# Kernel tuning notes

Measured on AMD Instinct MI355X. Metric: run time of the kernel, lower is better.

## Reference

```python
import jax, jax.numpy as jnp
import numpy as np

N_NODES = 100000
N_EDGES = 1600000
D_IN = 128
D_HID = 128
N_CLS = 2


def gcn_conv(x, edge_index, W, b):
    """PyG GCNConv: add self-loops, symmetric normalization, linear, scatter-add, bias."""
    n = x.shape[0]
    loop = jnp.arange(n, dtype=edge_index.dtype)
    src = jnp.concatenate([edge_index[0], loop])  # [E+N]
    dst = jnp.concatenate([edge_index[1], loop])
    # degree computed on destination (col) after adding self-loops
    deg = jax.ops.segment_sum(jnp.ones_like(dst, dtype=x.dtype), dst, num_segments=n)
    dinv = jnp.where(deg > 0, jax.lax.rsqrt(deg), 0.0)
    norm = dinv[src] * dinv[dst]  # [E+N]
    h = x @ W  # [N, out]
    msg = h[src] * norm[:, None]  # [E+N, out]
    out = jax.ops.segment_sum(msg, dst, num_segments=n)
    return out + b


def setup_inputs() -> dict:
    key = jax.random.key(0)
    k1, k2, k3, k4 = jax.random.split(key, 4)
    x = jax.random.normal(k1, (N_NODES, D_IN), dtype=jnp.float32)
    edge_index = jax.random.randint(k2, (2, N_EDGES), 0, N_NODES, dtype=jnp.int64)
    W1 = jax.random.normal(k3, (D_IN, D_HID), dtype=jnp.float32) * (1.0 / np.sqrt(D_IN))
    b1 = jnp.zeros((D_HID,), dtype=jnp.float32)
    W2 = jax.random.normal(k4, (D_HID, N_CLS), dtype=jnp.float32) * (1.0 / np.sqrt(D_HID))
    b2 = jnp.zeros((N_CLS,), dtype=jnp.float32)
    return {"x": x, "edge_index": edge_index, "W1": W1, "b1": b1, "W2": W2, "b2": b2}


def reference(x, edge_index, W1, b1, W2, b2):
    h = gcn_conv(x, edge_index, W1, b1)
    h = jax.nn.relu(h)
    # training=False -> dropout skipped
    out = gcn_conv(h, edge_index, W2, b2)
    return out
```

## Files before the change

kernel.cpp:

```cpp
#include <hip/hip_runtime.h>
#include <hip/hip_fp16.h>
#include <cstdint>
#include <cstddef>

#define NN 100000
#define NE 1600000
#define D 128
#define NBK 782
#define NBLK_P 200
#define EPB 8000
#define CAP 3072

typedef _Float16 half8 __attribute__((ext_vector_type(8)));
typedef _Float16 half4v __attribute__((ext_vector_type(4)));
typedef float f32x4 __attribute__((ext_vector_type(4)));


__launch_bounds__(256)
__global__ void pscat_k(const int* __restrict__ ei, unsigned* __restrict__ gcnt,
                        unsigned* __restrict__ part,
                        const float* __restrict__ W, _Float16* __restrict__ Wt) {
    __shared__ unsigned hist[NBK];
    __shared__ unsigned run[NBK];
    int tid = threadIdx.x, b = blockIdx.x;
    for (int k = tid; k < NBK; k += 256) hist[k] = 0u;
    __syncthreads();
    int e0 = b * EPB;
    for (int i = tid * 4; i < EPB; i += 1024) {
        int4 d4 = *(const int4*)(ei + NE + e0 + i);
        atomicAdd(&hist[d4.x >> 7], 1u);
        atomicAdd(&hist[d4.y >> 7], 1u);
        atomicAdd(&hist[d4.z >> 7], 1u);
        atomicAdd(&hist[d4.w >> 7], 1u);
    }
    __syncthreads();
    for (int k = tid; k < NBK; k += 256) {
        unsigned c = hist[k];
        run[k] = c ? atomicAdd(&gcnt[k * 16], c) : 0u;
    }
    if (b < 64) {
        int idx = b * 256 + tid;
        int n = idx >> 7, kk = idx & 127;
        Wt[idx] = (_Float16)W[kk * 128 + n];
    }
    __syncthreads();
    for (int i = tid * 4; i < EPB; i += 1024) {
        int4 s4 = *(const int4*)(ei + e0 + i);
        int4 d4 = *(const int4*)(ei + NE + e0 + i);
        unsigned k, slot;
        k = (unsigned)(d4.x >> 7); slot = atomicAdd(&run[k], 1u);
        if (slot < CAP) part[(size_t)k * CAP + slot] = (unsigned)s4.x | ((unsigned)(d4.x & 127) << 20);
        k = (unsigned)(d4.y >> 7); slot = atomicAdd(&run[k], 1u);
        if (slot < CAP) part[(size_t)k * CAP + slot] = (unsigned)s4.y | ((unsigned)(d4.y & 127) << 20);
        k = (unsigned)(d4.z >> 7); slot = atomicAdd(&run[k], 1u);
        if (slot < CAP) part[(size_t)k * CAP + slot] = (unsigned)s4.z | ((unsigned)(d4.z & 127) << 20);
        k = (unsigned)(d4.w >> 7); slot = atomicAdd(&run[k], 1u);
        if (slot < CAP) part[(size_t)k * CAP + slot] = (unsigned)s4.w | ((unsigned)(d4.w & 127) << 20);
    }
}

__global__ void pscan_k(const unsigned* __restrict__ gcnt, unsigned* __restrict__ base) {
    __shared__ unsigned sh[1024];
    int t = threadIdx.x;
    unsigned v = 0u;
    if (t < NBK) {
        v = gcnt[t * 16];
        if (v > CAP) v = CAP;
    }
    sh[t] = v;
    __syncthreads();
    for (int off = 1; off < 1024; off <<= 1) {
        unsigned u = (t >= off) ? sh[t - off] : 0u;
        __syncthreads();
        sh[t] += u;
        __syncthreads();
    }
    if (t < NBK) base[t] = sh[t] - v;
    if (t == NBK) base[NBK] = sh[NBK - 1];
}

__launch_bounds__(256)
__global__ void p4_csr_k(const unsigned* __restrict__ part, const unsigned* __restrict__ base,
                         unsigned* __restrict__ rp, float* __restrict__ dinv,
                         unsigned* __restrict__ col) {
    __shared__ unsigned c[128], p[128], run[128];
    int tid = threadIdx.x, k = blockIdx.x;
    int n0 = k << 7;
    int nodes = (NN - n0 < 128) ? (NN - n0) : 128;
    unsigned e0c = base[k], e1c = base[k + 1];
    unsigned cnt = e1c - e0c;
    const unsigned* pk = part + (size_t)k * CAP;

    if (tid < 128) c[tid] = 0u;
    __syncthreads();
    for (unsigned t = tid; t < cnt; t += 256)
        atomicAdd(&c[(pk[t] >> 20) & 127], 1u);
    __syncthreads();

    unsigned myc = (tid < 128) ? c[tid] : 0u;
    if (tid < 128) p[tid] = myc;
    __syncthreads();
    for (int off = 1; off < 128; off <<= 1) {
        unsigned u = 0;
        if (tid < 128 && tid >= off) u = p[tid - off];
        __syncthreads();
        if (tid < 128) p[tid] += u;
        __syncthreads();
    }
    if (tid < 128) {
        unsigned excl = p[tid] - myc;
        run[tid] = excl;
        if (tid < nodes) {
            rp[n0 + tid] = e0c + excl;
            dinv[n0 + tid] = rsqrtf((float)(myc + 1u));
        }
    }
    if (k == 0 && tid == 0) rp[NN] = base[NBK];
    __syncthreads();

    for (unsigned t = tid; t < cnt; t += 256) {
        unsigned v = pk[t];
        unsigned dlo = (v >> 20) & 127;
        unsigned pos = e0c + atomicAdd(&run[dlo], 1u);
        col[pos] = v & 0xFFFFFu;
    }
}

__launch_bounds__(256)
__global__ void gemm1_k(const float* __restrict__ x, const _Float16* __restrict__ Wt,
                        const float* __restrict__ dinv, _Float16* __restrict__ h) {
    __shared__ _Float16 wt[128 * 136];
    __shared__ _Float16 xs[128 * 72];
    int tid = threadIdx.x;
    int rb = blockIdx.x * 128;
    int w = tid >> 6, lane = tid & 63;
    int m = lane & 15, q4 = lane >> 4;

#pragma unroll
    for (int q = 0; q < 8; q++) {
        int idx = q * 256 + tid;
        int n = idx >> 4, k8 = (idx & 15) * 8;
        *(half8*)(&wt[n * 136 + k8]) = *(const half8*)(Wt + n * 128 + k8);
    }

    f32x4 acc[2][8];
#pragma unroll
    for (int rt = 0; rt < 2; rt++)
#pragma unroll
        for (int nt = 0; nt < 8; nt++) acc[rt][nt] = (f32x4){0.f, 0.f, 0.f, 0.f};

    for (int ks = 0; ks <= 64; ks += 64) {
        if (ks) __syncthreads();
#pragma unroll
        for (int q = 0; q < 8; q++) {
            int idx = q * 256 + tid;
            int row = idx >> 4;
            int c4 = (idx & 15) * 4;
            int gr = rb + row;
            float4 v = (gr < NN) ? *(const float4*)(x + (size_t)gr * 128 + ks + c4)
                                 : make_float4(0, 0, 0, 0);
            half4v hv = { (_Float16)v.x, (_Float16)v.y, (_Float16)v.z, (_Float16)v.w };
            *(half4v*)(&xs[row * 72 + c4]) = hv;
        }
        __syncthreads();

#pragma unroll
        for (int kc = 0; kc < 2; kc++) {
            half8 a0 = *(const half8*)(&xs[(w * 32 + m) * 72 + kc * 32 + q4 * 8]);
            half8 a1 = *(const half8*)(&xs[(w * 32 + 16 + m) * 72 + kc * 32 + q4 * 8]);
#pragma unroll
            for (int nt = 0; nt < 8; nt++) {
                half8 bf = *(const half8*)(&wt[(nt * 16 + m) * 136 + ks + kc * 32 + q4 * 8]);
                acc[0][nt] = __builtin_amdgcn_mfma_f32_16x16x32_f16(a0, bf, acc[0][nt], 0, 0, 0);
                acc[1][nt] = __builtin_amdgcn_mfma_f32_16x16x32_f16(a1, bf, acc[1][nt], 0, 0, 0);
            }
        }
    }

    float dv[2][4];
#pragma unroll
    for (int rt = 0; rt < 2; rt++)
#pragma unroll
        for (int r = 0; r < 4; r++) {
            int ri = rb + w * 32 + rt * 16 + q4 * 4 + r;
            dv[rt][r] = (ri < NN) ? dinv[ri] : 0.f;
        }
    __syncthreads();
#pragma unroll
    for (int rt = 0; rt < 2; rt++)
#pragma unroll
        for (int nt = 0; nt < 8; nt++)
#pragma unroll
            for (int r = 0; r < 4; r++)
                wt[(w * 32 + rt * 16 + q4 * 4 + r) * 136 + nt * 16 + m] =
                    (_Float16)(acc[rt][nt][r] * dv[rt][r]);
    __syncthreads();
#pragma unroll
    for (int q = 0; q < 8; q++) {
        int idx = q * 256 + tid;
        int row = idx >> 4;
        int c8 = (idx & 15) * 8;
        int gr = rb + row;
        if (gr < NN)
            *(half8*)(h + (size_t)gr * 128 + c8) = *(const half8*)(&wt[row * 136 + c8]);
    }
}

__launch_bounds__(256)
__global__ void agg1_k(const _Float16* __restrict__ h, const unsigned* __restrict__ rp,
                       const unsigned* __restrict__ col, const float* __restrict__ dinv,
                       const float* __restrict__ b1, const float* __restrict__ W2,
                       float* __restrict__ z, int nb, int ne) {
    int i = nb + ((blockIdx.x * 256 + threadIdx.x) >> 6);
    int lane = threadIdx.x & 63;
    if (i >= ne) return;
    unsigned si = __builtin_amdgcn_readfirstlane((unsigned)i);

    const __half2* hb = (const __half2*)h;
    unsigned p0 = __builtin_amdgcn_readfirstlane(rp[si]);
    unsigned p1 = __builtin_amdgcn_readfirstlane(rp[si + 1]);
    int deg = (int)(p1 - p0);

    unsigned cv = col[p0 + (unsigned)lane];

    int degc = deg > 64 ? 64 : deg;
    int R = (degc + 15) >> 4;
    float2 sv = __half22float2(hb[(size_t)si * 64u + lane]);
    float f = (float)(1 + degc - 16 * R);
    float ax = f * sv.x, ay = f * sv.y;

#define ROUND16(r)                                                           \
    {                                                                        \
        float2 vv[16];                                                       \
        _Pragma("unroll")                                                    \
        for (int t = 0; t < 16; t++) {                                       \
            int k = (r) * 16 + t;                                            \
            unsigned s = (k < degc) ? __builtin_amdgcn_readlane(cv, k) : si; \
            vv[t] = __half22float2(hb[(size_t)s * 64u + lane]);              \
        }                                                                    \
        ax += ((vv[0].x + vv[1].x) + (vv[2].x + vv[3].x))                    \
            + ((vv[4].x + vv[5].x) + (vv[6].x + vv[7].x))                    \
            + ((vv[8].x + vv[9].x) + (vv[10].x + vv[11].x))                  \
            + ((vv[12].x + vv[13].x) + (vv[14].x + vv[15].x));               \
        ay += ((vv[0].y + vv[1].y) + (vv[2].y + vv[3].y))                    \
            + ((vv[4].y + vv[5].y) + (vv[6].y + vv[7].y))                    \
            + ((vv[8].y + vv[9].y) + (vv[10].y + vv[11].y))                  \
            + ((vv[12].y + vv[13].y) + (vv[14].y + vv[15].y));               \
    }

    if (degc > 0)  ROUND16(0)
    if (degc > 16) ROUND16(1)
    if (degc > 32) ROUND16(2)
    if (degc > 48) ROUND16(3)
#undef ROUND16

    for (unsigned e = p0 + 64; e < p1; ++e) {
        unsigned s_ = __builtin_amdgcn_readfirstlane(col[e]);
        float2 v = __half22float2(hb[(size_t)s_ * 64u + lane]);
        ax += v.x;
        ay += v.y;
    }

    float di = dinv[si];
    ax *= di;
    ay *= di;

    float2 bv = ((const float2*)b1)[lane];
    float h0 = fmaxf(ax + bv.x, 0.f);
    float h1 = fmaxf(ay + bv.y, 0.f);

    float4 w = ((const float4*)W2)[lane];
    float pz0 = fmaf(h0, w.x, h1 * w.z);
    float pz1 = fmaf(h0, w.y, h1 * w.w);
#pragma unroll
    for (int off = 32; off > 0; off >>= 1) {
        pz0 += __shfl_down(pz0, off);
        pz1 += __shfl_down(pz1, off);
    }
    if (lane == 0) {
        float2* zp = (float2*)(z + (size_t)si * 2);
        *zp = make_float2(pz0 * di, pz1 * di);
    }
}

__launch_bounds__(256)
__global__ void agg2_k(const float* __restrict__ z, const unsigned* __restrict__ rp,
                       const unsigned* __restrict__ col, const float* __restrict__ dinv,
                       const float* __restrict__ b2, float* __restrict__ out) {
    int i = (blockIdx.x * 256 + threadIdx.x) >> 4;
    int sl = threadIdx.x & 15;
    if (i >= NN) return;

    unsigned p0 = rp[i], p1 = rp[i + 1];
    float a0 = 0.f, a1 = 0.f;
    for (unsigned e = p0 + sl; e < p1; e += 16) {
        unsigned s = col[e];
        float2 v = ((const float2*)z)[s];
        a0 += v.x;
        a1 += v.y;
    }
#pragma unroll
    for (int off = 8; off > 0; off >>= 1) {
        a0 += __shfl_down(a0, off, 16);
        a1 += __shfl_down(a1, off, 16);
    }
    if (sl == 0) {
        float di = dinv[i];
        float2 zi = ((const float2*)z)[i];
        out[(size_t)i * 2]     = (a0 + zi.x) * di + b2[0];
        out[(size_t)i * 2 + 1] = (a1 + zi.y) * di + b2[1];
    }
}

extern "C" void kernel_launch(void* const* d_in, const int* in_sizes, int n_in,
                              void* d_out, int out_size, void* d_ws, size_t ws_size,
                              hipStream_t stream) {
    const float* x  = (const float*)d_in[0];
    const int*   ei = (const int*)d_in[1];
    const float* W1 = (const float*)d_in[2];
    const float* b1 = (const float*)d_in[3];
    const float* W2 = (const float*)d_in[4];
    const float* b2 = (const float*)d_in[5];
    float* out = (float*)d_out;

    char* ws = (char*)d_ws;
    unsigned* part = (unsigned*)(ws);
    unsigned* gcnt = (unsigned*)(ws + 9609216);
    unsigned* base = (unsigned*)(ws + 9659264);
    _Float16* h    = (_Float16*)(ws);
    float*    z    = (float*)(ws + 25600000);
    float*    dinv = (float*)(ws + 26400000);
    unsigned* rp   = (unsigned*)(ws + 26800000);
    unsigned* col  = (unsigned*)(ws + 27200016);
    _Float16* Wt   = (_Float16*)(ws + 33600016);

    hipMemsetAsync(gcnt, 0, 782 * 16 * sizeof(unsigned), stream);
    pscat_k<<<NBLK_P, 256, 0, stream>>>(ei, gcnt, part, W1, Wt);
    pscan_k<<<1, 1024, 0, stream>>>(gcnt, base);
    p4_csr_k<<<NBK, 256, 0, stream>>>(part, base, rp, dinv, col);

    gemm1_k<<<(NN + 127) / 128, 256, 0, stream>>>(x, Wt, dinv, h);
    agg1_k<<<(50000 * 64 + 255) / 256, 256, 0, stream>>>(h, rp, col, dinv, b1, W2, z, 0, 50000);
    agg1_k<<<(50000 * 64 + 255) / 256, 256, 0, stream>>>(h, rp, col, dinv, b1, W2, z, 50000, NN);
    agg2_k<<<(NN * 16 + 255) / 256, 256, 0, stream>>>(z, rp, col, dinv, b2, out);
}
```

Before: 227.0 us.

## Split layer-1 aggregation across two feature halves with interleaved block mapping

The first-layer gather is restructured so that each wavefront handles only 64 of the 128 hidden features of a node, loading one half per lane instead of a half2. Block IDs are interleaved so that nearby blocks cover both halves of the same node group, keeping the gathered rows' cache lines hot. Each half writes its own partial layer-2 projection (z0, z1), and agg2 sums the two. This doubles the number of wavefronts and the neighbor-index work. It also replaces the two half-range launches with a single launch, aiming for more parallelism and better L2 locality. The cost is twice the z reads in agg2 and narrower 2-byte loads per lane.

```diff
diff --git a/kernel.cpp b/kernel.cpp
--- a/kernel.cpp
+++ b/kernel.cpp
@@ -207,16 +207,24 @@
 }
 
 __launch_bounds__(256)
-__global__ void agg1_k(const _Float16* __restrict__ h, const unsigned* __restrict__ rp,
-                       const unsigned* __restrict__ col, const float* __restrict__ dinv,
-                       const float* __restrict__ b1, const float* __restrict__ W2,
-                       float* __restrict__ z, int nb, int ne) {
-    int i = nb + ((blockIdx.x * 256 + threadIdx.x) >> 6);
+__global__ void agg1h_k(const _Float16* __restrict__ h, const unsigned* __restrict__ rp,
+                        const unsigned* __restrict__ col, const float* __restrict__ dinv,
+                        const float* __restrict__ b1, const float* __restrict__ W2,
+                        float* __restrict__ z0, float* __restrict__ z1) {
+    unsigned bid = blockIdx.x;
+    unsigned rr = bid & 7u, q = bid >> 3;
+    unsigned dh = rr >> 2;
+    unsigned g  = q * 4u + (rr & 3u);
+    int wv = threadIdx.x >> 6;
     int lane = threadIdx.x & 63;
-    if (i >= ne) return;
-    unsigned si = __builtin_amdgcn_readfirstlane((unsigned)i);
-
-    const __half2* hb = (const __half2*)h;
+    unsigned i = g * 4u + (unsigned)wv;
+    if (i >= NN) return;
+    unsigned si = __builtin_amdgcn_readfirstlane(i);
+
+    const __half* hh = (const __half*)h;
+    unsigned doff = dh * 64u + (unsigned)lane;
+    const __half* hd = hh + doff;
+
     unsigned p0 = __builtin_amdgcn_readfirstlane(rp[si]);
     unsigned p1 = __builtin_amdgcn_readfirstlane(rp[si + 1]);
     int deg = (int)(p1 - p0);
@@ -225,27 +233,23 @@
 
     int degc = deg > 64 ? 64 : deg;
     int R = (degc + 15) >> 4;
-    float2 sv = __half22float2(hb[(size_t)si * 64u + lane]);
+    float sv = __half2float(hd[(size_t)si * 128u]);
     float f = (float)(1 + degc - 16 * R);
-    float ax = f * sv.x, ay = f * sv.y;
+    float ax = f * sv;
 
 #define ROUND16(r)                                                           \
     {                                                                        \
-        float2 vv[16];                                                       \
+        float vv[16];                                                        \
         _Pragma("unroll")                                                    \
         for (int t = 0; t < 16; t++) {                                       \
             int k = (r) * 16 + t;                                            \
             unsigned s = (k < degc) ? __builtin_amdgcn_readlane(cv, k) : si; \
-            vv[t] = __half22float2(hb[(size_t)s * 64u + lane]);              \
+            vv[t] = __half2float(hd[(size_t)s * 128u]);                      \
         }                                                                    \
-        ax += ((vv[0].x + vv[1].x) + (vv[2].x + vv[3].x))                    \
-            + ((vv[4].x + vv[5].x) + (vv[6].x + vv[7].x))                    \
-            + ((vv[8].x + vv[9].x) + (vv[10].x + vv[11].x))                  \
-            + ((vv[12].x + vv[13].x) + (vv[14].x + vv[15].x));               \
-        ay += ((vv[0].y + vv[1].y) + (vv[2].y + vv[3].y))                    \
-            + ((vv[4].y + vv[5].y) + (vv[6].y + vv[7].y))                    \
-            + ((vv[8].y + vv[9].y) + (vv[10].y + vv[11].y))                  \
-            + ((vv[12].y + vv[13].y) + (vv[14].y + vv[15].y));               \
+        ax += (((vv[0] + vv[1]) + (vv[2] + vv[3]))                           \
+             + ((vv[4] + vv[5]) + (vv[6] + vv[7])))                          \
+            + (((vv[8] + vv[9]) + (vv[10] + vv[11]))                         \
+             + ((vv[12] + vv[13]) + (vv[14] + vv[15])));                     \
     }
 
     if (degc > 0)  ROUND16(0)
@@ -256,37 +260,31 @@
 
     for (unsigned e = p0 + 64; e < p1; ++e) {
         unsigned s_ = __builtin_amdgcn_readfirstlane(col[e]);
-        float2 v = __half22float2(hb[(size_t)s_ * 64u + lane]);
-        ax += v.x;
-        ay += v.y;
+        ax += __half2float(hd[(size_t)s_ * 128u]);
     }
 
     float di = dinv[si];
-    ax *= di;
-    ay *= di;
-
-    float2 bv = ((const float2*)b1)[lane];
-    float h0 = fmaxf(ax + bv.x, 0.f);
-    float h1 = fmaxf(ay + bv.y, 0.f);
-
-    float4 w = ((const float4*)W2)[lane];
-    float pz0 = fmaf(h0, w.x, h1 * w.z);
-    float pz1 = fmaf(h0, w.y, h1 * w.w);
+    float h0 = fmaxf(fmaf(ax, di, b1[doff]), 0.f);
+
+    float2 w = ((const float2*)W2)[doff];
+    float pz0 = h0 * w.x;
+    float pz1 = h0 * w.y;
 #pragma unroll
     for (int off = 32; off > 0; off >>= 1) {
         pz0 += __shfl_down(pz0, off);
         pz1 += __shfl_down(pz1, off);
     }
     if (lane == 0) {
-        float2* zp = (float2*)(z + (size_t)si * 2);
-        *zp = make_float2(pz0 * di, pz1 * di);
-    }
-}
-
-__launch_bounds__(256)
-__global__ void agg2_k(const float* __restrict__ z, const unsigned* __restrict__ rp,
-                       const unsigned* __restrict__ col, const float* __restrict__ dinv,
-                       const float* __restrict__ b2, float* __restrict__ out) {
+        float* zp = (dh ? z1 : z0) + (size_t)si * 2;
+        *(float2*)zp = make_float2(pz0 * di, pz1 * di);
+    }
+}
+
+__launch_bounds__(256)
+__global__ void agg2_k(const float* __restrict__ z0, const float* __restrict__ z1,
+                       const unsigned* __restrict__ rp, const unsigned* __restrict__ col,
+                       const float* __restrict__ dinv, const float* __restrict__ b2,
+                       float* __restrict__ out) {
     int i = (blockIdx.x * 256 + threadIdx.x) >> 4;
     int sl = threadIdx.x & 15;
     if (i >= NN) return;
@@ -295,9 +293,10 @@
     float a0 = 0.f, a1 = 0.f;
     for (unsigned e = p0 + sl; e < p1; e += 16) {
         unsigned s = col[e];
-        float2 v = ((const float2*)z)[s];
-        a0 += v.x;
-        a1 += v.y;
+        float2 va = ((const float2*)z0)[s];
+        float2 vb = ((const float2*)z1)[s];
+        a0 += va.x + vb.x;
+        a1 += va.y + vb.y;
     }
 #pragma unroll
     for (int off = 8; off > 0; off >>= 1) {
@@ -306,9 +305,10 @@
     }
     if (sl == 0) {
         float di = dinv[i];
-        float2 zi = ((const float2*)z)[i];
-        out[(size_t)i * 2]     = (a0 + zi.x) * di + b2[0];
-        out[(size_t)i * 2 + 1] = (a1 + zi.y) * di + b2[1];
+        float2 za = ((const float2*)z0)[i];
+        float2 zb = ((const float2*)z1)[i];
+        out[(size_t)i * 2]     = (a0 + za.x + zb.x) * di + b2[0];
+        out[(size_t)i * 2 + 1] = (a1 + za.y + zb.y) * di + b2[1];
     }
 }
 
@@ -328,11 +328,12 @@
     unsigned* gcnt = (unsigned*)(ws + 9609216);
     unsigned* base = (unsigned*)(ws + 9659264);
     _Float16* h    = (_Float16*)(ws);
-    float*    z    = (float*)(ws + 25600000);
+    float*    z0   = (float*)(ws + 25600000);
     float*    dinv = (float*)(ws + 26400000);
     unsigned* rp   = (unsigned*)(ws + 26800000);
     unsigned* col  = (unsigned*)(ws + 27200016);
     _Float16* Wt   = (_Float16*)(ws + 33600016);
+    float*    z1   = (float*)(ws + 33632784);
 
     hipMemsetAsync(gcnt, 0, 782 * 16 * sizeof(unsigned), stream);
     pscat_k<<<NBLK_P, 256, 0, stream>>>(ei, gcnt, part, W1, Wt);
@@ -340,7 +341,6 @@
     p4_csr_k<<<NBK, 256, 0, stream>>>(part, base, rp, dinv, col);
 
     gemm1_k<<<(NN + 127) / 128, 256, 0, stream>>>(x, Wt, dinv, h);
-    agg1_k<<<(50000 * 64 + 255) / 256, 256, 0, stream>>>(h, rp, col, dinv, b1, W2, z, 0, 50000);
-    agg1_k<<<(50000 * 64 + 255) / 256, 256, 0, stream>>>(h, rp, col, dinv, b1, W2, z, 50000, NN);
-    agg2_k<<<(NN * 16 + 255) / 256, 256, 0, stream>>>(z, rp, col, dinv, b2, out);
-}
+    agg1h_k<<<50000, 256, 0, stream>>>(h, rp, col, dinv, b1, W2, z0, z1);
+    agg2_k<<<(NN * 16 + 255) / 256, 256, 0, stream>>>(z0, z1, rp, col, dinv, b2, out);
+}
```

Measured after the change: 344.7 us. 1.52x slower.
